# Kernel tuning notes

Measured on AMD Instinct MI355X. Metric: run time of the kernel, lower is better.

The kernel has to match this reference:

```python
import jax, jax.numpy as jnp
import numpy as np

B, S, D, H = 4, 2048, 1024, 16
DH = D // H  # 64


def setup_inputs() -> dict:
    key = jax.random.key(0)
    ks = jax.random.split(key, 7)
    scale = 1.0 / np.sqrt(DH)
    return {
        "elements": jax.random.normal(ks[0], (B, S, D), dtype=jnp.float32),
        # per-head Linear(d_head, d_head): weight [H, DH, DH] (out, in), bias [H, DH]
        "Wq": jax.random.normal(ks[1], (H, DH, DH), dtype=jnp.float32) * scale,
        "bq": jax.random.normal(ks[2], (H, DH), dtype=jnp.float32) * 0.01,
        "Wk": jax.random.normal(ks[3], (H, DH, DH), dtype=jnp.float32) * scale,
        "bk": jax.random.normal(ks[4], (H, DH), dtype=jnp.float32) * 0.01,
        "Wv": jax.random.normal(ks[5], (H, DH, DH), dtype=jnp.float32) * scale,
        "bv": jax.random.normal(ks[6], (H, DH), dtype=jnp.float32) * 0.01,
    }


def reference(elements, Wq, bq, Wk, bk, Wv, bv):
    b, s, d = elements.shape
    x = elements.reshape(b, s, H, DH)  # head-sliced channels
    # nn.Linear: y = x @ W.T + b, per head
    q = jnp.einsum("bshd,hed->bshe", x, Wq) + bq
    k = jnp.einsum("bshd,hed->bshe", x, Wk) + bk
    v = jnp.einsum("bshd,hed->bshe", x, Wv) + bv
    # NOTE: original scales by sqrt(nb_heads), not sqrt(d_head)
    scores = jnp.einsum("bshd,bthd->bhst", q, k) / jnp.sqrt(jnp.float32(H))
    attn = jax.nn.softmax(scores, axis=-1)
    out = jnp.einsum("bhst,bthd->bshd", attn, v)
    return out.reshape(b, s, d)
```

## Files before the change

kernel.cpp:

```cpp
#include <hip/hip_runtime.h>
#include <hip/hip_bf16.h>

#define BB 4
#define SS 2048
#define DD 1024
#define HH 16

typedef short bf16x8 __attribute__((ext_vector_type(8)));
typedef float f32x4 __attribute__((ext_vector_type(4)));
typedef float f32x16 __attribute__((ext_vector_type(16)));
typedef unsigned int uint32x4 __attribute__((ext_vector_type(4)));
typedef unsigned short u16x4 __attribute__((ext_vector_type(4)));

__device__ __forceinline__ unsigned short f2bf(float f) {
  __hip_bfloat16 h = __float2bfloat16(f);
  return __builtin_bit_cast(unsigned short, h);
}
__device__ __forceinline__ unsigned int pack2(float a, float b) {
  return (unsigned int)f2bf(a) | ((unsigned int)f2bf(b) << 16);
}

__global__ __launch_bounds__(256) void qkv_proj(
    const float* __restrict__ x,
    const float* __restrict__ Wq, const float* __restrict__ bq,
    const float* __restrict__ Wk, const float* __restrict__ bk,
    const float* __restrict__ Wv, const float* __restrict__ bv,
    unsigned short* __restrict__ Q, unsigned short* __restrict__ K,
    unsigned short* __restrict__ Vt)
{
  const float QSC = 0.25f * 1.44269504088896f;
  int bid = blockIdx.x;
  int bh = bid & 63;
  int sbg = bid >> 6;
  int h = bh & (HH - 1);
  int b = bh >> 4;
  int t = threadIdx.x;
  int w = t >> 6, lane = t & 63;
  int g = lane >> 4, c = lane & 15;

  bf16x8 wqf[4][2], wkf[4][2], wvf[4][2];
#pragma unroll
  for (int et = 0; et < 4; ++et) {
#pragma unroll
    for (int kk = 0; kk < 2; ++kk) {
      int e = 16 * et + c;
      int d0 = 32 * kk + 8 * g;
      const float4* pq = reinterpret_cast<const float4*>(Wq + (h * 64 + e) * 64 + d0);
      const float4* pk = reinterpret_cast<const float4*>(Wk + (h * 64 + e) * 64 + d0);
      const float4* pv = reinterpret_cast<const float4*>(Wv + (h * 64 + e) * 64 + d0);
      float4 q0 = pq[0], q1 = pq[1];
      float4 k0 = pk[0], k1 = pk[1];
      float4 v0 = pv[0], v1 = pv[1];
      bf16x8 aq, ak, av;
      aq[0] = (short)f2bf(QSC * q0.x); aq[1] = (short)f2bf(QSC * q0.y);
      aq[2] = (short)f2bf(QSC * q0.z); aq[3] = (short)f2bf(QSC * q0.w);
      aq[4] = (short)f2bf(QSC * q1.x); aq[5] = (short)f2bf(QSC * q1.y);
      aq[6] = (short)f2bf(QSC * q1.z); aq[7] = (short)f2bf(QSC * q1.w);
      ak[0] = (short)f2bf(k0.x); ak[1] = (short)f2bf(k0.y);
      ak[2] = (short)f2bf(k0.z); ak[3] = (short)f2bf(k0.w);
      ak[4] = (short)f2bf(k1.x); ak[5] = (short)f2bf(k1.y);
      ak[6] = (short)f2bf(k1.z); ak[7] = (short)f2bf(k1.w);
      av[0] = (short)f2bf(v0.x); av[1] = (short)f2bf(v0.y);
      av[2] = (short)f2bf(v0.z); av[3] = (short)f2bf(v0.w);
      av[4] = (short)f2bf(v1.x); av[5] = (short)f2bf(v1.y);
      av[6] = (short)f2bf(v1.z); av[7] = (short)f2bf(v1.w);
      wqf[et][kk] = aq; wkf[et][kk] = ak; wvf[et][kk] = av;
    }
  }

  f32x4 bqv[4], bkv[4];
  float bvv[4];
#pragma unroll
  for (int et = 0; et < 4; ++et) {
#pragma unroll
    for (int r = 0; r < 4; ++r) {
      bqv[et][r] = QSC * bq[h * 64 + 16 * et + 4 * g + r];
      bkv[et][r] = bk[h * 64 + 16 * et + 4 * g + r];
    }
    bvv[et] = bv[h * 64 + 16 * et + c];
  }

  for (int i = 0; i < 4; ++i) {
    int s0 = (sbg * 4 + i) * 64 + w * 16;
    const float* xp = x + ((size_t)b * SS + s0 + c) * DD + h * 64;
    bf16x8 xf[2];
#pragma unroll
    for (int kk = 0; kk < 2; ++kk) {
      const float4* px = reinterpret_cast<const float4*>(xp + 32 * kk + 8 * g);
      float4 x0 = px[0], x1 = px[1];
      bf16x8 a;
      a[0] = (short)f2bf(x0.x); a[1] = (short)f2bf(x0.y);
      a[2] = (short)f2bf(x0.z); a[3] = (short)f2bf(x0.w);
      a[4] = (short)f2bf(x1.x); a[5] = (short)f2bf(x1.y);
      a[6] = (short)f2bf(x1.z); a[7] = (short)f2bf(x1.w);
      xf[kk] = a;
    }

    size_t qsrow = ((size_t)bh * SS + s0 + c) * 64;
#pragma unroll
    for (int et = 0; et < 4; ++et) {
      f32x4 aq = bqv[et];
      f32x4 ak = bkv[et];
      aq = __builtin_amdgcn_mfma_f32_16x16x32_bf16(wqf[et][0], xf[0], aq, 0, 0, 0);
      aq = __builtin_amdgcn_mfma_f32_16x16x32_bf16(wqf[et][1], xf[1], aq, 0, 0, 0);
      ak = __builtin_amdgcn_mfma_f32_16x16x32_bf16(wkf[et][0], xf[0], ak, 0, 0, 0);
      ak = __builtin_amdgcn_mfma_f32_16x16x32_bf16(wkf[et][1], xf[1], ak, 0, 0, 0);
      u16x4 pq, pk;
#pragma unroll
      for (int r = 0; r < 4; ++r) { pq[r] = f2bf(aq[r]); pk[r] = f2bf(ak[r]); }
      *reinterpret_cast<u16x4*>(Q + qsrow + 16 * et + 4 * g) = pq;
      *reinterpret_cast<u16x4*>(K + qsrow + 16 * et + 4 * g) = pk;
    }

#pragma unroll
    for (int et = 0; et < 4; ++et) {
      f32x4 av = {bvv[et], bvv[et], bvv[et], bvv[et]};
      av = __builtin_amdgcn_mfma_f32_16x16x32_bf16(xf[0], wvf[et][0], av, 0, 0, 0);
      av = __builtin_amdgcn_mfma_f32_16x16x32_bf16(xf[1], wvf[et][1], av, 0, 0, 0);
      u16x4 pv;
#pragma unroll
      for (int r = 0; r < 4; ++r) pv[r] = f2bf(av[r]);
      *reinterpret_cast<u16x4*>(
          Vt + ((size_t)bh * 64 + 16 * et + c) * SS + s0 + 4 * g) = pv;
    }
  }
}

__global__ __launch_bounds__(256) void attn_fused(
    const unsigned short* __restrict__ Q, const unsigned short* __restrict__ K,
    const unsigned short* __restrict__ Vt, float* __restrict__ out)
{
  __shared__ unsigned short Kl[64 * 64];
  __shared__ unsigned short Vl[64 * 64];

  const int bid = blockIdx.x;
  const int bh = bid & 63;
  const int qblk = bid >> 6;
  const int t = threadIdx.x;
  const int w = t >> 6, lane = t & 63;
  const int c = lane & 31, hi = lane >> 5;

  const unsigned short* Qp = Q + ((size_t)bh * SS + qblk * 128 + w * 32 + c) * 64;
  bf16x8 qf[4];
#pragma unroll
  for (int ks = 0; ks < 4; ++ks)
    qf[ks] = *reinterpret_cast<const bf16x8*>(Qp + ks * 16 + 8 * hi);

  const unsigned short* Kp = K + (size_t)bh * SS * 64;
  const unsigned short* Vp = Vt + (size_t)bh * 64 * SS;

  f32x16 oacc[2];
#pragma unroll
  for (int dt = 0; dt < 2; ++dt)
#pragma unroll
    for (int r = 0; r < 16; ++r) oacc[dt][r] = 0.f;
  float lsum = 0.f;

  int srow[2], sdst[2], ssrc[2];
#pragma unroll
  for (int i = 0; i < 2; ++i) {
    int ci = t + 256 * i;
    int row = ci >> 3, seg = ci & 7;
    int gsw = (seg ^ (row & 7) ^ (row >> 3)) & 7;
    srow[i] = row; sdst[i] = row * 64 + gsw * 8; ssrc[i] = seg * 8;
  }

  bf16x8 kreg[2], vreg[2];
#pragma unroll
  for (int i = 0; i < 2; ++i) {
    kreg[i] = *reinterpret_cast<const bf16x8*>(Kp + (size_t)srow[i] * 64 + ssrc[i]);
    vreg[i] = *reinterpret_cast<const bf16x8*>(Vp + (size_t)srow[i] * SS + ssrc[i]);
  }

  for (int kv0 = 0; kv0 < SS; kv0 += 64) {
#pragma unroll
    for (int i = 0; i < 2; ++i) {
      *reinterpret_cast<bf16x8*>(Kl + sdst[i]) = kreg[i];
      *reinterpret_cast<bf16x8*>(Vl + sdst[i]) = vreg[i];
    }
    __syncthreads();

    if (kv0 + 64 < SS) {
#pragma unroll
      for (int i = 0; i < 2; ++i) {
        kreg[i] = *reinterpret_cast<const bf16x8*>(
            Kp + (size_t)(kv0 + 64 + srow[i]) * 64 + ssrc[i]);
        vreg[i] = *reinterpret_cast<const bf16x8*>(
            Vp + (size_t)srow[i] * SS + kv0 + 64 + ssrc[i]);
      }
    }

    f32x16 sacc[2];
#pragma unroll
    for (int st = 0; st < 2; ++st)
#pragma unroll
      for (int r = 0; r < 16; ++r) sacc[st][r] = 0.f;
#pragma unroll
    for (int st = 0; st < 2; ++st) {
      int row = st * 32 + c;
      int swz = ((row & 7) ^ (row >> 3)) & 7;
#pragma unroll
      for (int ks = 0; ks < 4; ++ks) {
        bf16x8 kf = *reinterpret_cast<const bf16x8*>(
            Kl + row * 64 + (((2 * ks + hi) ^ swz) & 7) * 8);
        sacc[st] = __builtin_amdgcn_mfma_f32_32x32x16_bf16(kf, qf[ks], sacc[st], 0, 0, 0);
      }
    }

    float p[2][16];
    float psum = 0.f;
#pragma unroll
    for (int st = 0; st < 2; ++st)
#pragma unroll
      for (int r = 0; r < 16; ++r) {
        float v = __builtin_amdgcn_exp2f(sacc[st][r]);
        p[st][r] = v; psum += v;
      }
    psum += __shfl_xor(psum, 32);
    lsum += psum;

    unsigned int Wd[2][4][2];
#pragma unroll
    for (int st = 0; st < 2; ++st)
#pragma unroll
      for (int qd = 0; qd < 4; ++qd) {
        Wd[st][qd][0] = pack2(p[st][4 * qd + 0], p[st][4 * qd + 1]);
        Wd[st][qd][1] = pack2(p[st][4 * qd + 2], p[st][4 * qd + 3]);
      }

    bf16x8 pfrag[4];
#pragma unroll
    for (int ks = 0; ks < 4; ++ks) {
      int sti = ks >> 1, qd0 = 2 * (ks & 1);
      unsigned int s0 = hi ? Wd[sti][qd0][0] : Wd[sti][qd0 + 1][0];
      unsigned int s1 = hi ? Wd[sti][qd0][1] : Wd[sti][qd0 + 1][1];
      unsigned int r0 = (unsigned int)__shfl_xor((int)s0, 32);
      unsigned int r1 = (unsigned int)__shfl_xor((int)s1, 32);
      uint32x4 wv;
      wv[0] = hi ? r0 : Wd[sti][qd0][0];
      wv[1] = hi ? r1 : Wd[sti][qd0][1];
      wv[2] = hi ? Wd[sti][qd0 + 1][0] : r0;
      wv[3] = hi ? Wd[sti][qd0 + 1][1] : r1;
      pfrag[ks] = __builtin_bit_cast(bf16x8, wv);
    }

#pragma unroll
    for (int dt = 0; dt < 2; ++dt) {
      int row = dt * 32 + c;
      int swz = ((row & 7) ^ (row >> 3)) & 7;
#pragma unroll
      for (int ks = 0; ks < 4; ++ks) {
        bf16x8 vf = *reinterpret_cast<const bf16x8*>(
            Vl + row * 64 + (((2 * ks + hi) ^ swz) & 7) * 8);
        oacc[dt] = __builtin_amdgcn_mfma_f32_32x32x16_bf16(pfrag[ks], vf, oacc[dt], 0, 0, 0);
      }
    }
    __syncthreads();
  }

  const int b = bh >> 4, h = bh & (HH - 1);
  float* op = out + ((size_t)b * SS + qblk * 128 + w * 32) * DD + h * 64;
#pragma unroll
  for (int r = 0; r < 16; ++r) {
    int orow = (r & 3) + 8 * (r >> 2) + 4 * hi;
    float linv = 1.f / __shfl(lsum, orow);
    op[(size_t)orow * DD + c]      = oacc[0][r] * linv;
    op[(size_t)orow * DD + 32 + c] = oacc[1][r] * linv;
  }
}

extern "C" void kernel_launch(void* const* d_in, const int* in_sizes, int n_in,
                              void* d_out, int out_size, void* d_ws, size_t ws_size,
                              hipStream_t stream) {
  const float* x  = (const float*)d_in[0];
  const float* Wq = (const float*)d_in[1];
  const float* bq = (const float*)d_in[2];
  const float* Wk = (const float*)d_in[3];
  const float* bk = (const float*)d_in[4];
  const float* Wv = (const float*)d_in[5];
  const float* bv = (const float*)d_in[6];
  float* out = (float*)d_out;

  unsigned short* ws = (unsigned short*)d_ws;
  const size_t per = (size_t)BB * HH * SS * 64;
  unsigned short* Q  = ws;
  unsigned short* K  = ws + per;
  unsigned short* Vt = ws + 2 * per;

  qkv_proj<<<(BB * HH) * 8, 256, 0, stream>>>(x, Wq, bq, Wk, bk, Wv, bv, Q, K, Vt);
  attn_fused<<<(SS / 128) * (BB * HH), 256, 0, stream>>>(Q, K, Vt, out);
}
```

Before: 217.3 us.

## Widen attention query tiles, double-buffer K/V via direct LDS loads, coalesce QKV stores

Each wave in the attention kernel now handles two 32-row query subtiles. K/V fragments are read from LDS once and reused for both, so the grid halves. K/V tiles are staged with global_load_lds into a double-buffered swizzled LDS area, replacing the register round-trip prefetch. The projection kernel writes Q, K and the transposed V through LDS so global stores become full 16-byte coalesced rows, at the cost of extra barriers. The larger per-wave tile raises register pressure and leaves fewer blocks to spread across CUs.

```diff
diff --git a/kernel.cpp b/kernel.cpp
--- a/kernel.cpp
+++ b/kernel.cpp
@@ -18,6 +18,11 @@
 }
 __device__ __forceinline__ unsigned int pack2(float a, float b) {
   return (unsigned int)f2bf(a) | ((unsigned int)f2bf(b) << 16);
+}
+__device__ __forceinline__ void gl16(const unsigned short* g, unsigned short* l) {
+  __builtin_amdgcn_global_load_lds(
+      (const __attribute__((address_space(1))) void*)g,
+      (__attribute__((address_space(3))) void*)l, 16, 0, 0);
 }
 
 __global__ __launch_bounds__(256) void qkv_proj(
@@ -28,6 +33,10 @@
     unsigned short* __restrict__ Q, unsigned short* __restrict__ K,
     unsigned short* __restrict__ Vt)
 {
+  __shared__ unsigned short Ql[64 * 64];
+  __shared__ unsigned short Kl2[64 * 64];
+  __shared__ unsigned short Vl2[64 * 64];
+
   const float QSC = 0.25f * 1.44269504088896f;
   int bid = blockIdx.x;
   int bh = bid & 63;
@@ -81,7 +90,8 @@
   }
 
   for (int i = 0; i < 4; ++i) {
-    int s0 = (sbg * 4 + i) * 64 + w * 16;
+    int sblk = (sbg * 4 + i) * 64;
+    int s0 = sblk + w * 16;
     const float* xp = x + ((size_t)b * SS + s0 + c) * DD + h * 64;
     bf16x8 xf[2];
 #pragma unroll
@@ -96,7 +106,7 @@
       xf[kk] = a;
     }
 
-    size_t qsrow = ((size_t)bh * SS + s0 + c) * 64;
+    int sl = w * 16 + c;
 #pragma unroll
     for (int et = 0; et < 4; ++et) {
       f32x4 aq = bqv[et];
@@ -108,8 +118,10 @@
       u16x4 pq, pk;
 #pragma unroll
       for (int r = 0; r < 4; ++r) { pq[r] = f2bf(aq[r]); pk[r] = f2bf(ak[r]); }
-      *reinterpret_cast<u16x4*>(Q + qsrow + 16 * et + 4 * g) = pq;
-      *reinterpret_cast<u16x4*>(K + qsrow + 16 * et + 4 * g) = pk;
+      int g16 = 2 * et + (g >> 1), lo = g & 1;
+      int off = sl * 64 + ((g16 ^ (sl & 7)) * 8) + lo * 4;
+      *reinterpret_cast<u16x4*>(Ql + off) = pq;
+      *reinterpret_cast<u16x4*>(Kl2 + off) = pk;
     }
 
 #pragma unroll
@@ -120,9 +132,27 @@
       u16x4 pv;
 #pragma unroll
       for (int r = 0; r < 4; ++r) pv[r] = f2bf(av[r]);
-      *reinterpret_cast<u16x4*>(
-          Vt + ((size_t)bh * 64 + 16 * et + c) * SS + s0 + 4 * g) = pv;
-    }
+      int re = 16 * et + c;
+      int g16 = 2 * w + (g >> 1), lo = g & 1;
+      int off = re * 64 + ((g16 ^ (re & 7)) * 8) + lo * 4;
+      *reinterpret_cast<u16x4*>(Vl2 + off) = pv;
+    }
+    __syncthreads();
+
+    size_t qkbase = ((size_t)bh * SS + sblk) * 64;
+#pragma unroll
+    for (int jj = 0; jj < 2; ++jj) {
+      int idx = t + 256 * jj;
+      int row = idx >> 3, g16 = idx & 7;
+      int loff = row * 64 + ((g16 ^ (row & 7)) * 8);
+      bf16x8 qv = *reinterpret_cast<const bf16x8*>(Ql + loff);
+      bf16x8 kv = *reinterpret_cast<const bf16x8*>(Kl2 + loff);
+      bf16x8 vv = *reinterpret_cast<const bf16x8*>(Vl2 + loff);
+      *reinterpret_cast<bf16x8*>(Q + qkbase + (size_t)idx * 8) = qv;
+      *reinterpret_cast<bf16x8*>(K + qkbase + (size_t)idx * 8) = kv;
+      *reinterpret_cast<bf16x8*>(Vt + ((size_t)bh * 64 + row) * SS + sblk + g16 * 8) = vv;
+    }
+    __syncthreads();
   }
 }
 
@@ -130,142 +160,151 @@
     const unsigned short* __restrict__ Q, const unsigned short* __restrict__ K,
     const unsigned short* __restrict__ Vt, float* __restrict__ out)
 {
-  __shared__ unsigned short Kl[64 * 64];
-  __shared__ unsigned short Vl[64 * 64];
+  __shared__ unsigned short KLb[2][64 * 64];
+  __shared__ unsigned short VLb[2][64 * 64];
 
   const int bid = blockIdx.x;
   const int bh = bid & 63;
-  const int qblk = bid >> 6;
+  const int qpan = bid >> 6;
   const int t = threadIdx.x;
   const int w = t >> 6, lane = t & 63;
   const int c = lane & 31, hi = lane >> 5;
-
-  const unsigned short* Qp = Q + ((size_t)bh * SS + qblk * 128 + w * 32 + c) * 64;
-  bf16x8 qf[4];
-#pragma unroll
-  for (int ks = 0; ks < 4; ++ks)
-    qf[ks] = *reinterpret_cast<const bf16x8*>(Qp + ks * 16 + 8 * hi);
+  const int lrow = lane >> 3, lg = lane & 7;
+
+  const unsigned short* Qp = Q + ((size_t)bh * SS + qpan * 256 + w * 64 + c) * 64;
+  bf16x8 qf[2][4];
+#pragma unroll
+  for (int qs = 0; qs < 2; ++qs)
+#pragma unroll
+    for (int ks = 0; ks < 4; ++ks)
+      qf[qs][ks] = *reinterpret_cast<const bf16x8*>(
+          Qp + qs * 32 * 64 + ks * 16 + 8 * hi);
 
   const unsigned short* Kp = K + (size_t)bh * SS * 64;
   const unsigned short* Vp = Vt + (size_t)bh * 64 * SS;
 
-  f32x16 oacc[2];
-#pragma unroll
-  for (int dt = 0; dt < 2; ++dt)
-#pragma unroll
-    for (int r = 0; r < 16; ++r) oacc[dt][r] = 0.f;
-  float lsum = 0.f;
-
-  int srow[2], sdst[2], ssrc[2];
-#pragma unroll
-  for (int i = 0; i < 2; ++i) {
-    int ci = t + 256 * i;
-    int row = ci >> 3, seg = ci & 7;
-    int gsw = (seg ^ (row & 7) ^ (row >> 3)) & 7;
-    srow[i] = row; sdst[i] = row * 64 + gsw * 8; ssrc[i] = seg * 8;
-  }
-
-  bf16x8 kreg[2], vreg[2];
-#pragma unroll
-  for (int i = 0; i < 2; ++i) {
-    kreg[i] = *reinterpret_cast<const bf16x8*>(Kp + (size_t)srow[i] * 64 + ssrc[i]);
-    vreg[i] = *reinterpret_cast<const bf16x8*>(Vp + (size_t)srow[i] * SS + ssrc[i]);
-  }
-
-  for (int kv0 = 0; kv0 < SS; kv0 += 64) {
-#pragma unroll
-    for (int i = 0; i < 2; ++i) {
-      *reinterpret_cast<bf16x8*>(Kl + sdst[i]) = kreg[i];
-      *reinterpret_cast<bf16x8*>(Vl + sdst[i]) = vreg[i];
-    }
-    __syncthreads();
-
-    if (kv0 + 64 < SS) {
-#pragma unroll
-      for (int i = 0; i < 2; ++i) {
-        kreg[i] = *reinterpret_cast<const bf16x8*>(
-            Kp + (size_t)(kv0 + 64 + srow[i]) * 64 + ssrc[i]);
-        vreg[i] = *reinterpret_cast<const bf16x8*>(
-            Vp + (size_t)srow[i] * SS + kv0 + 64 + ssrc[i]);
-      }
-    }
-
-    f32x16 sacc[2];
-#pragma unroll
-    for (int st = 0; st < 2; ++st)
-#pragma unroll
-      for (int r = 0; r < 16; ++r) sacc[st][r] = 0.f;
+  f32x16 oacc[2][2];
+#pragma unroll
+  for (int qs = 0; qs < 2; ++qs)
+#pragma unroll
+    for (int dt = 0; dt < 2; ++dt)
+#pragma unroll
+      for (int r = 0; r < 16; ++r) oacc[qs][dt][r] = 0.f;
+  float lsum[2] = {0.f, 0.f};
+
+#define STAGE(KV0, BUF)                                                        \
+  {                                                                            \
+    int kv0_ = (KV0);                                                          \
+    _Pragma("unroll")                                                          \
+    for (int i = 0; i < 2; ++i) {                                              \
+      int row = w * 16 + i * 8 + lrow;                                         \
+      int src = (lg ^ (row & 7) ^ (row >> 3)) & 7;                             \
+      gl16(Kp + (size_t)(kv0_ + row) * 64 + src * 8,                           \
+           &KLb[BUF][(w * 16 + i * 8) * 64]);                                  \
+      gl16(Vp + (size_t)row * SS + kv0_ + src * 8,                             \
+           &VLb[BUF][(w * 16 + i * 8) * 64]);                                  \
+    }                                                                          \
+  }
+
+  STAGE(0, 0);
+  __syncthreads();
+  int cur = 0;
+
+  for (int t32 = 0; t32 < SS / 64; ++t32) {
+    if (t32 + 1 < SS / 64) STAGE((t32 + 1) * 64, cur ^ 1);
+    const unsigned short* Kl = KLb[cur];
+    const unsigned short* Vl = VLb[cur];
+
+    bf16x8 kfr[2][4], vfr[2][4];
 #pragma unroll
     for (int st = 0; st < 2; ++st) {
       int row = st * 32 + c;
       int swz = ((row & 7) ^ (row >> 3)) & 7;
 #pragma unroll
-      for (int ks = 0; ks < 4; ++ks) {
-        bf16x8 kf = *reinterpret_cast<const bf16x8*>(
+      for (int ks = 0; ks < 4; ++ks)
+        kfr[st][ks] = *reinterpret_cast<const bf16x8*>(
             Kl + row * 64 + (((2 * ks + hi) ^ swz) & 7) * 8);
-        sacc[st] = __builtin_amdgcn_mfma_f32_32x32x16_bf16(kf, qf[ks], sacc[st], 0, 0, 0);
-      }
-    }
-
-    float p[2][16];
-    float psum = 0.f;
-#pragma unroll
-    for (int st = 0; st < 2; ++st)
-#pragma unroll
-      for (int r = 0; r < 16; ++r) {
-        float v = __builtin_amdgcn_exp2f(sacc[st][r]);
-        p[st][r] = v; psum += v;
-      }
-    psum += __shfl_xor(psum, 32);
-    lsum += psum;
-
-    unsigned int Wd[2][4][2];
-#pragma unroll
-    for (int st = 0; st < 2; ++st)
-#pragma unroll
-      for (int qd = 0; qd < 4; ++qd) {
-        Wd[st][qd][0] = pack2(p[st][4 * qd + 0], p[st][4 * qd + 1]);
-        Wd[st][qd][1] = pack2(p[st][4 * qd + 2], p[st][4 * qd + 3]);
-      }
-
-    bf16x8 pfrag[4];
-#pragma unroll
-    for (int ks = 0; ks < 4; ++ks) {
-      int sti = ks >> 1, qd0 = 2 * (ks & 1);
-      unsigned int s0 = hi ? Wd[sti][qd0][0] : Wd[sti][qd0 + 1][0];
-      unsigned int s1 = hi ? Wd[sti][qd0][1] : Wd[sti][qd0 + 1][1];
-      unsigned int r0 = (unsigned int)__shfl_xor((int)s0, 32);
-      unsigned int r1 = (unsigned int)__shfl_xor((int)s1, 32);
-      uint32x4 wv;
-      wv[0] = hi ? r0 : Wd[sti][qd0][0];
-      wv[1] = hi ? r1 : Wd[sti][qd0][1];
-      wv[2] = hi ? Wd[sti][qd0 + 1][0] : r0;
-      wv[3] = hi ? Wd[sti][qd0 + 1][1] : r1;
-      pfrag[ks] = __builtin_bit_cast(bf16x8, wv);
-    }
-
+    }
 #pragma unroll
     for (int dt = 0; dt < 2; ++dt) {
       int row = dt * 32 + c;
       int swz = ((row & 7) ^ (row >> 3)) & 7;
 #pragma unroll
+      for (int ks = 0; ks < 4; ++ks)
+        vfr[dt][ks] = *reinterpret_cast<const bf16x8*>(
+            Vl + row * 64 + (((2 * ks + hi) ^ swz) & 7) * 8);
+    }
+
+#pragma unroll
+    for (int qs = 0; qs < 2; ++qs) {
+      f32x16 sacc[2];
+#pragma unroll
+      for (int st = 0; st < 2; ++st)
+#pragma unroll
+        for (int r = 0; r < 16; ++r) sacc[st][r] = 0.f;
+#pragma unroll
+      for (int st = 0; st < 2; ++st)
+#pragma unroll
+        for (int ks = 0; ks < 4; ++ks)
+          sacc[st] = __builtin_amdgcn_mfma_f32_32x32x16_bf16(
+              kfr[st][ks], qf[qs][ks], sacc[st], 0, 0, 0);
+
+      float psum = 0.f;
+      unsigned int Wd[2][4][2];
+#pragma unroll
+      for (int st = 0; st < 2; ++st)
+#pragma unroll
+        for (int qd = 0; qd < 4; ++qd) {
+          float p0 = __builtin_amdgcn_exp2f(sacc[st][4 * qd + 0]);
+          float p1 = __builtin_amdgcn_exp2f(sacc[st][4 * qd + 1]);
+          float p2 = __builtin_amdgcn_exp2f(sacc[st][4 * qd + 2]);
+          float p3 = __builtin_amdgcn_exp2f(sacc[st][4 * qd + 3]);
+          psum += (p0 + p1) + (p2 + p3);
+          Wd[st][qd][0] = pack2(p0, p1);
+          Wd[st][qd][1] = pack2(p2, p3);
+        }
+      psum += __shfl_xor(psum, 32);
+      lsum[qs] += psum;
+
+      bf16x8 pfrag[4];
+#pragma unroll
       for (int ks = 0; ks < 4; ++ks) {
-        bf16x8 vf = *reinterpret_cast<const bf16x8*>(
-            Vl + row * 64 + (((2 * ks + hi) ^ swz) & 7) * 8);
-        oacc[dt] = __builtin_amdgcn_mfma_f32_32x32x16_bf16(pfrag[ks], vf, oacc[dt], 0, 0, 0);
+        int sti = ks >> 1, qd0 = 2 * (ks & 1);
+        unsigned int s0 = hi ? Wd[sti][qd0][0] : Wd[sti][qd0 + 1][0];
+        unsigned int s1 = hi ? Wd[sti][qd0][1] : Wd[sti][qd0 + 1][1];
+        unsigned int r0 = (unsigned int)__shfl_xor((int)s0, 32);
+        unsigned int r1 = (unsigned int)__shfl_xor((int)s1, 32);
+        uint32x4 wv;
+        wv[0] = hi ? r0 : Wd[sti][qd0][0];
+        wv[1] = hi ? r1 : Wd[sti][qd0][1];
+        wv[2] = hi ? Wd[sti][qd0 + 1][0] : r0;
+        wv[3] = hi ? Wd[sti][qd0 + 1][1] : r1;
+        pfrag[ks] = __builtin_bit_cast(bf16x8, wv);
       }
-    }
+
+#pragma unroll
+      for (int dt = 0; dt < 2; ++dt)
+#pragma unroll
+        for (int ks = 0; ks < 4; ++ks)
+          oacc[qs][dt] = __builtin_amdgcn_mfma_f32_32x32x16_bf16(
+              pfrag[ks], vfr[dt][ks], oacc[qs][dt], 0, 0, 0);
+    }
+
     __syncthreads();
+    cur ^= 1;
   }
 
   const int b = bh >> 4, h = bh & (HH - 1);
-  float* op = out + ((size_t)b * SS + qblk * 128 + w * 32) * DD + h * 64;
-#pragma unroll
-  for (int r = 0; r < 16; ++r) {
-    int orow = (r & 3) + 8 * (r >> 2) + 4 * hi;
-    float linv = 1.f / __shfl(lsum, orow);
-    op[(size_t)orow * DD + c]      = oacc[0][r] * linv;
-    op[(size_t)orow * DD + 32 + c] = oacc[1][r] * linv;
+#pragma unroll
+  for (int qs = 0; qs < 2; ++qs) {
+    float* op = out + ((size_t)b * SS + qpan * 256 + w * 64 + qs * 32) * DD + h * 64;
+#pragma unroll
+    for (int r = 0; r < 16; ++r) {
+      int orow = (r & 3) + 8 * (r >> 2) + 4 * hi;
+      float linv = 1.f / __shfl(lsum[qs], orow);
+      op[(size_t)orow * DD + c]      = oacc[qs][0][r] * linv;
+      op[(size_t)orow * DD + 32 + c] = oacc[qs][1][r] * linv;
+    }
   }
 }
 
@@ -288,5 +327,5 @@
   unsigned short* Vt = ws + 2 * per;
 
   qkv_proj<<<(BB * HH) * 8, 256, 0, stream>>>(x, Wq, bq, Wk, bk, Wv, bv, Q, K, Vt);
-  attn_fused<<<(SS / 128) * (BB * HH), 256, 0, stream>>>(Q, K, Vt, out);
-}
+  attn_fused<<<(SS / 256) * (BB * HH), 256, 0, stream>>>(Q, K, Vt, out);
+}
```

Result: slower. 240.4 us (+10.7%).
